# Optimization experiments

Measured on AMD Instinct MI355X. Metric: run time of the kernel, lower is better.

The kernel has to match this reference:

```python
import jax, jax.numpy as jnp
import numpy as np

ALPHA = 0.2   # LeakyReLU negative slope
NEG = -1e9    # mask value for non-edges


def setup_inputs() -> dict:
    key = jax.random.key(0)
    ks = jax.random.split(key, 8)
    N, Din, F, H, Dout = 4096, 512, 64, 8, 16
    adj = (jax.random.uniform(ks[0], (N, N)) < 0.01).astype(jnp.float32)
    adjacency = jnp.maximum(adj, jnp.eye(N, dtype=jnp.float32))
    X = jax.random.normal(ks[1], (N, Din), jnp.float32)
    s = lambda k, shape, fan: jax.random.normal(k, shape, jnp.float32) / np.float32(np.sqrt(fan))
    W = s(ks[2], (H, Din, F), Din)        # per-head projection, stacked
    a1 = s(ks[3], (H, F), F)              # attention vector, source half
    a2 = s(ks[4], (H, F), F)              # attention vector, target half
    Wo = s(ks[5], (H * F, Dout), H * F)   # output-layer projection
    ao1 = s(ks[6], (Dout,), Dout)
    ao2 = s(ks[7], (Dout,), Dout)
    return dict(adjacency=adjacency, X=X, W=W, a1=a1, a2=a2, Wo=Wo, ao1=ao1, ao2=ao2)


def reference(adjacency, X, W, a1, a2, Wo, ao1, ao2):
    # dropout is identity (eval mode / p=0)
    mask = adjacency > 0
    N = X.shape[0]
    # --- multi-head attention layers (concat=True -> ELU) ---
    Wh = jnp.einsum('nd,hdf->hnf', X, W)                      # [H, N, F]
    f1 = jnp.einsum('hnf,hf->hn', Wh, a1)                     # [H, N]
    f2 = jnp.einsum('hnf,hf->hn', Wh, a2)                     # [H, N]
    e = jax.nn.leaky_relu(f1[:, :, None] + f2[:, None, :], ALPHA)  # [H, N, N]
    att = jax.nn.softmax(jnp.where(mask[None], e, NEG), axis=-1)
    heads = jax.nn.elu(jnp.einsum('hnm,hmf->hnf', att, Wh))   # [H, N, F]
    cat = jnp.transpose(heads, (1, 0, 2)).reshape(N, -1)      # [N, H*F]
    # --- output attention layer (concat=False -> no ELU) ---
    Who = cat @ Wo                                            # [N, Dout]
    eo = jax.nn.leaky_relu((Who @ ao1)[:, None] + (Who @ ao2)[None, :], ALPHA)
    atto = jax.nn.softmax(jnp.where(mask, eo, NEG), axis=-1)  # [N, N]
    return atto @ Who                                         # [N, Dout]
```

## Files before the change

kernel.cpp:

```cpp
#include <hip/hip_runtime.h>
#include <hip/hip_bf16.h>

#define N_NODES 4096
#define DIN     512
#define FDIM    64
#define NHEADS  8
#define DOUT    16
#define MAXN    512

typedef __attribute__((ext_vector_type(8))) short bf16x8;
typedef __attribute__((ext_vector_type(4))) float f32x4;

static __device__ __forceinline__ float us2f(unsigned short u) {
    union { unsigned int i; float f; } cv; cv.i = ((unsigned int)u) << 16; return cv.f;
}
static __device__ __forceinline__ unsigned short f2us(float v) {
    __hip_bfloat16 b = __float2bfloat16(v);
    return *(const unsigned short*)&b;
}
static __device__ __forceinline__ int is_f32(const void* adj) {
    return (((const unsigned short*)adj)[0] == 0) ? 1 : 0;
}

__global__ __launch_bounds__(256) void prep_nbr_kernel(
    const void* __restrict__ adj, const void* __restrict__ X, const void* __restrict__ W,
    const void* __restrict__ a1, const void* __restrict__ a2, const void* __restrict__ Wo,
    const void* __restrict__ ao1, const void* __restrict__ ao2,
    unsigned short* __restrict__ Xb, unsigned short* __restrict__ Wt,
    unsigned short* __restrict__ WtH, unsigned short* __restrict__ WtL,
    float* __restrict__ a1c, float* __restrict__ a2c,
    float* __restrict__ ao1c, float* __restrict__ ao2c,
    int* __restrict__ cnt, int* __restrict__ nbr)
{
    const int f32 = is_f32(adj);
    if (blockIdx.x >= 1024) {
        const int n = blockIdx.x - 1024;
        __shared__ int c;
        if (threadIdx.x == 0) c = 0;
        __syncthreads();
        if (f32) {
            const uint4* row = (const uint4*)((const unsigned int*)adj + (size_t)n * N_NODES);
            for (int q = threadIdx.x; q < N_NODES / 4; q += 256) {
                uint4 v = row[q];
                int base = q * 4;
                if (v.x) { int p = atomicAdd(&c, 1); if (p < MAXN) nbr[(size_t)n * MAXN + p] = base + 0; }
                if (v.y) { int p = atomicAdd(&c, 1); if (p < MAXN) nbr[(size_t)n * MAXN + p] = base + 1; }
                if (v.z) { int p = atomicAdd(&c, 1); if (p < MAXN) nbr[(size_t)n * MAXN + p] = base + 2; }
                if (v.w) { int p = atomicAdd(&c, 1); if (p < MAXN) nbr[(size_t)n * MAXN + p] = base + 3; }
            }
        } else {
            const ushort4* row = (const ushort4*)((const unsigned short*)adj + (size_t)n * N_NODES);
            for (int q = threadIdx.x; q < N_NODES / 4; q += 256) {
                ushort4 v = row[q];
                int base = q * 4;
                if (v.x) { int p = atomicAdd(&c, 1); if (p < MAXN) nbr[(size_t)n * MAXN + p] = base + 0; }
                if (v.y) { int p = atomicAdd(&c, 1); if (p < MAXN) nbr[(size_t)n * MAXN + p] = base + 1; }
                if (v.z) { int p = atomicAdd(&c, 1); if (p < MAXN) nbr[(size_t)n * MAXN + p] = base + 2; }
                if (v.w) { int p = atomicAdd(&c, 1); if (p < MAXN) nbr[(size_t)n * MAXN + p] = base + 3; }
            }
        }
        __syncthreads();
        if (threadIdx.x == 0) cnt[n] = (c < MAXN) ? c : MAXN;
        return;
    }
    const int i0 = blockIdx.x * 256 + threadIdx.x;
    const int T = 1024 * 256;
    for (int i = i0; i < N_NODES * DIN; i += T) {
        float v = f32 ? ((const float*)X)[i] : us2f(((const unsigned short*)X)[i]);
        Xb[i] = f2us(v);
    }
    for (int i = i0; i < NHEADS * DIN * FDIM; i += T) {
        int hh = i >> 15, rem = i & 32767, d = rem >> 6, f = rem & 63;
        float v = f32 ? ((const float*)W)[i] : us2f(((const unsigned short*)W)[i]);
        Wt[((size_t)(hh * FDIM + f)) * DIN + d] = f2us(v);
    }
    for (int i = i0; i < DIN * DOUT; i += T) {
        int d = i >> 4, j = i & 15;
        float v = f32 ? ((const float*)Wo)[i] : us2f(((const unsigned short*)Wo)[i]);
        unsigned short hi = f2us(v);
        WtH[j * DIN + d] = hi;
        WtL[j * DIN + d] = f2us(v - us2f(hi));
    }
    if (i0 < 512) {
        a1c[i0] = f32 ? ((const float*)a1)[i0] : us2f(((const unsigned short*)a1)[i0]);
        a2c[i0] = f32 ? ((const float*)a2)[i0] : us2f(((const unsigned short*)a2)[i0]);
    }
    if (i0 < 16) {
        ao1c[i0] = f32 ? ((const float*)ao1)[i0] : us2f(((const unsigned short*)ao1)[i0]);
        ao2c[i0] = f32 ? ((const float*)ao2)[i0] : us2f(((const unsigned short*)ao2)[i0]);
    }
}

__global__ __launch_bounds__(256) void wh_f12_kernel(
    const unsigned short* __restrict__ Xb, const unsigned short* __restrict__ Wt,
    const float* __restrict__ a1c, const float* __restrict__ a2c,
    unsigned short* __restrict__ Whb, float* __restrict__ f1, float* __restrict__ f2)
{
    const int h  = blockIdx.x;
    const int bm = blockIdx.y;
    const int w    = threadIdx.x >> 6;
    const int lane = threadIdx.x & 63;
    const int quad = lane >> 4;
    const int l16  = lane & 15;
    const int rowA = bm * 64 + w * 16 + l16;

    f32x4 acc[4];
#pragma unroll
    for (int j = 0; j < 4; ++j) acc[j] = (f32x4){0.f, 0.f, 0.f, 0.f};

    const unsigned short* xp = Xb + (size_t)rowA * DIN + quad * 8;
    const unsigned short* wb = Wt + (size_t)h * FDIM * DIN + quad * 8;
#pragma unroll 4
    for (int k0 = 0; k0 < DIN; k0 += 32) {
        bf16x8 a = *(const bf16x8*)(xp + k0);
#pragma unroll
        for (int j = 0; j < 4; ++j) {
            bf16x8 b = *(const bf16x8*)(wb + (size_t)(j * 16 + l16) * DIN + k0);
            acc[j] = __builtin_amdgcn_mfma_f32_16x16x32_bf16(a, b, acc[j], 0, 0, 0);
        }
    }
    float av1[4], av2[4];
#pragma unroll
    for (int j = 0; j < 4; ++j) {
        int col = j * 16 + l16;
        av1[j] = a1c[h * FDIM + col];
        av2[j] = a2c[h * FDIM + col];
#pragma unroll
        for (int rr = 0; rr < 4; ++rr) {
            int row = bm * 64 + w * 16 + quad * 4 + rr;
            Whb[((size_t)row * NHEADS + h) * FDIM + col] = f2us(acc[j][rr]);
        }
    }
#pragma unroll
    for (int rr = 0; rr < 4; ++rr) {
        float p1 = acc[0][rr] * av1[0] + acc[1][rr] * av1[1] + acc[2][rr] * av1[2] + acc[3][rr] * av1[3];
        float p2 = acc[0][rr] * av2[0] + acc[1][rr] * av2[1] + acc[2][rr] * av2[2] + acc[3][rr] * av2[3];
#pragma unroll
        for (int off = 8; off; off >>= 1) {
            p1 += __shfl_xor(p1, off);
            p2 += __shfl_xor(p2, off);
        }
        if (l16 == 0) {
            int row = bm * 64 + w * 16 + quad * 4 + rr;
            f1[h * N_NODES + row] = p1;
            f2[h * N_NODES + row] = p2;
        }
    }
}

__global__ __launch_bounds__(256) void attn1_kernel(
    const unsigned short* __restrict__ Whb,
    const float* __restrict__ f1, const float* __restrict__ f2,
    const int* __restrict__ cnt, const int* __restrict__ nbr,
    unsigned short* __restrict__ catb)
{
    const int n = blockIdx.x;
    const int tid = threadIdx.x;
    __shared__ int sh_m[MAXN];
    __shared__ float sh_s[NHEADS][516];
    __shared__ float sh_inv[NHEADS];
    const int c0 = cnt[n];
    const int c = (c0 < MAXN) ? c0 : MAXN;
    for (int k = tid; k < c; k += 256) sh_m[k] = nbr[(size_t)n * MAXN + k];
    __syncthreads();
    const int h = tid >> 5;
    const int l32 = tid & 31;
    const float f1v = f1[h * N_NODES + n];
    float mx = -1e30f;
    for (int k = l32; k < c; k += 32) {
        float s = f1v + f2[h * N_NODES + sh_m[k]];
        s = (s >= 0.f) ? s : 0.2f * s;
        sh_s[h][k] = s;
        mx = fmaxf(mx, s);
    }
#pragma unroll
    for (int off = 16; off; off >>= 1) mx = fmaxf(mx, __shfl_xor(mx, off));
    __syncthreads();
    float sum = 0.f;
    for (int k = l32; k < c; k += 32) {
        float e = __expf(sh_s[h][k] - mx);
        sh_s[h][k] = e;
        sum += e;
    }
#pragma unroll
    for (int off = 16; off; off >>= 1) sum += __shfl_xor(sum, off);
    if (l32 == 0) sh_inv[h] = (sum > 0.f) ? 1.f / sum : 0.f;
    __syncthreads();
    float a0 = 0.f, a1v = 0.f;
    const unsigned int* base = (const unsigned int*)Whb;
#pragma unroll 8
    for (int k = 0; k < c; ++k) {
        unsigned int u = base[(size_t)sh_m[k] * 256 + tid];
        float wgt = sh_s[h][k];
        a0  += wgt * us2f((unsigned short)(u & 0xFFFFu));
        a1v += wgt * us2f((unsigned short)(u >> 16));
    }
    const float inv = sh_inv[h];
    a0 *= inv; a1v *= inv;
    a0  = (a0  > 0.f) ? a0  : expm1f(a0);
    a1v = (a1v > 0.f) ? a1v : expm1f(a1v);
    unsigned int o = (unsigned int)f2us(a0) | ((unsigned int)f2us(a1v) << 16);
    ((unsigned int*)catb)[(size_t)n * 256 + tid] = o;
}

__global__ __launch_bounds__(64) void who_mfma_g_kernel(
    const unsigned short* __restrict__ catb,
    const unsigned short* __restrict__ WtH, const unsigned short* __restrict__ WtL,
    const float* __restrict__ ao1c, const float* __restrict__ ao2c,
    float* __restrict__ Who, float* __restrict__ g1, float* __restrict__ g2)
{
    const int lane = threadIdx.x;
    const int quad = lane >> 4, l16 = lane & 15;
    const int row0 = blockIdx.x * 16;
    f32x4 acc = (f32x4){0.f, 0.f, 0.f, 0.f};
    for (int k0 = 0; k0 < DIN; k0 += 32) {
        bf16x8 a  = *(const bf16x8*)&catb[(size_t)(row0 + l16) * DIN + k0 + quad * 8];
        bf16x8 bh = *(const bf16x8*)&WtH[l16 * DIN + k0 + quad * 8];
        bf16x8 bl = *(const bf16x8*)&WtL[l16 * DIN + k0 + quad * 8];
        acc = __builtin_amdgcn_mfma_f32_16x16x32_bf16(a, bh, acc, 0, 0, 0);
        acc = __builtin_amdgcn_mfma_f32_16x16x32_bf16(a, bl, acc, 0, 0, 0);
    }
#pragma unroll
    for (int rr = 0; rr < 4; ++rr) {
        int row = row0 + quad * 4 + rr;
        float v = acc[rr];
        Who[row * DOUT + l16] = v;
        float p1 = v * ao1c[l16];
        float p2 = v * ao2c[l16];
#pragma unroll
        for (int off = 8; off; off >>= 1) {
            p1 += __shfl_xor(p1, off);
            p2 += __shfl_xor(p2, off);
        }
        if (l16 == 0) { g1[row] = p1; g2[row] = p2; }
    }
}

__global__ __launch_bounds__(64) void attn2_kernel(
    const void* __restrict__ adj,
    const float* __restrict__ Who,
    const float* __restrict__ g1, const float* __restrict__ g2,
    const int* __restrict__ cnt, const int* __restrict__ nbr,
    void* __restrict__ out)
{
    const int n = blockIdx.x;
    const int lane = threadIdx.x;
    const int quad = lane >> 4, l16 = lane & 15;
    __shared__ float sh_s[MAXN];
    __shared__ int sh_m[MAXN];
    const int c0 = cnt[n];
    const int c = (c0 < MAXN) ? c0 : MAXN;
    for (int k = lane; k < c; k += 64) sh_m[k] = nbr[(size_t)n * MAXN + k];
    __syncthreads();
    const float gn = g1[n];
    float mx = -1e30f;
    for (int k = lane; k < c; k += 64) {
        float s = gn + g2[sh_m[k]];
        s = (s >= 0.f) ? s : 0.2f * s;
        sh_s[k] = s;
        mx = fmaxf(mx, s);
    }
#pragma unroll
    for (int off = 32; off; off >>= 1) mx = fmaxf(mx, __shfl_xor(mx, off));
    __syncthreads();
    float sum = 0.f;
    for (int k = lane; k < c; k += 64) {
        float e = __expf(sh_s[k] - mx);
        sh_s[k] = e;
        sum += e;
    }
#pragma unroll
    for (int off = 32; off; off >>= 1) sum += __shfl_xor(sum, off);
    __syncthreads();
    const float inv = (sum > 0.f) ? 1.f / sum : 0.f;
    float accv = 0.f;
#pragma unroll 4
    for (int k = quad; k < c; k += 4)
        accv += sh_s[k] * Who[sh_m[k] * DOUT + l16];
    accv += __shfl_xor(accv, 16);
    accv += __shfl_xor(accv, 32);
    if (quad == 0) {
        float v = accv * inv;
        if (is_f32(adj)) ((float*)out)[n * DOUT + l16] = v;
        else             ((unsigned short*)out)[n * DOUT + l16] = f2us(v);
    }
}

__global__ void wsfail_kernel(float* __restrict__ out)
{
    if (threadIdx.x == 0) out[0] = 129.f;
}

extern "C" void kernel_launch(void* const* d_in, const int* in_sizes, int n_in,
                              void* d_out, int out_size, void* d_ws, size_t ws_size,
                              hipStream_t stream)
{
    const void* adj = d_in[0];
    const void* X   = d_in[1];
    const void* W   = d_in[2];
    const void* a1  = d_in[3];
    const void* a2  = d_in[4];
    const void* Wo  = d_in[5];
    const void* ao1 = d_in[6];
    const void* ao2 = d_in[7];

    const size_t NEEDED = 22000000;
    if (ws_size < NEEDED) { wsfail_kernel<<<1, 64, 0, stream>>>((float*)d_out); return; }

    int*   cnt  = (int*)d_ws;
    int*   nbr  = cnt + 4096;
    float* a1c  = (float*)(nbr + 2097152);
    float* a2c  = a1c + 512;
    float* ao1c = a2c + 512;
    float* ao2c = ao1c + 16;
    float* f1   = ao2c + 16;
    float* f2   = f1 + 32768;
    float* Who  = f2 + 32768;
    float* g1   = Who + 65536;
    float* g2   = g1 + 4096;
    unsigned short* Whb  = (unsigned short*)(g2 + 4096);
    unsigned short* catb = Whb + 2097152;
    unsigned short* Xb   = catb + 2097152;
    unsigned short* Wt   = Xb + 2097152;
    unsigned short* WtH  = Wt + 262144;
    unsigned short* WtL  = WtH + 8192;

    prep_nbr_kernel<<<1024 + N_NODES, 256, 0, stream>>>(
        adj, X, W, a1, a2, Wo, ao1, ao2,
        Xb, Wt, WtH, WtL, a1c, a2c, ao1c, ao2c, cnt, nbr);
    wh_f12_kernel<<<dim3(NHEADS, N_NODES / 64), 256, 0, stream>>>(
        Xb, Wt, a1c, a2c, Whb, f1, f2);
    attn1_kernel<<<N_NODES, 256, 0, stream>>>(Whb, f1, f2, cnt, nbr, catb);
    who_mfma_g_kernel<<<N_NODES / 16, 64, 0, stream>>>(catb, WtH, WtL, ao1c, ao2c, Who, g1, g2);
    attn2_kernel<<<N_NODES, 64, 0, stream>>>(adj, Who, g1, g2, cnt, nbr, d_out);
}
```

Baseline: 162.4 us.

## Fuse neighbor scan, head aggregation and output projection into attention kernel

Moves the per-row adjacency scan out of the prep kernel and into the first attention kernel, which keeps the neighbor list in shared memory and writes it out for the second layer. The output projection (cat @ Wo plus the g1/g2 dot products) is now done per node inside the same kernel in fp32, which removes the catb round trip and the separate MFMA kernel. The aggregation loop is restructured so each wave handles a different neighbor and loads 16-byte vectors, followed by a cross-wave shared-memory reduction. The wh_f12 MFMA operands are swapped so each lane stores contiguous features with a vector store. The fused kernel gains shared memory and a scalar per-node projection that may lower occupancy.

```diff
diff --git a/kernel.cpp b/kernel.cpp
--- a/kernel.cpp
+++ b/kernel.cpp
@@ -22,47 +22,16 @@
     return (((const unsigned short*)adj)[0] == 0) ? 1 : 0;
 }
 
-__global__ __launch_bounds__(256) void prep_nbr_kernel(
+__global__ __launch_bounds__(256) void prep_kernel(
     const void* __restrict__ adj, const void* __restrict__ X, const void* __restrict__ W,
     const void* __restrict__ a1, const void* __restrict__ a2, const void* __restrict__ Wo,
     const void* __restrict__ ao1, const void* __restrict__ ao2,
     unsigned short* __restrict__ Xb, unsigned short* __restrict__ Wt,
-    unsigned short* __restrict__ WtH, unsigned short* __restrict__ WtL,
+    float* __restrict__ Woc,
     float* __restrict__ a1c, float* __restrict__ a2c,
-    float* __restrict__ ao1c, float* __restrict__ ao2c,
-    int* __restrict__ cnt, int* __restrict__ nbr)
+    float* __restrict__ ao1c, float* __restrict__ ao2c)
 {
     const int f32 = is_f32(adj);
-    if (blockIdx.x >= 1024) {
-        const int n = blockIdx.x - 1024;
-        __shared__ int c;
-        if (threadIdx.x == 0) c = 0;
-        __syncthreads();
-        if (f32) {
-            const uint4* row = (const uint4*)((const unsigned int*)adj + (size_t)n * N_NODES);
-            for (int q = threadIdx.x; q < N_NODES / 4; q += 256) {
-                uint4 v = row[q];
-                int base = q * 4;
-                if (v.x) { int p = atomicAdd(&c, 1); if (p < MAXN) nbr[(size_t)n * MAXN + p] = base + 0; }
-                if (v.y) { int p = atomicAdd(&c, 1); if (p < MAXN) nbr[(size_t)n * MAXN + p] = base + 1; }
-                if (v.z) { int p = atomicAdd(&c, 1); if (p < MAXN) nbr[(size_t)n * MAXN + p] = base + 2; }
-                if (v.w) { int p = atomicAdd(&c, 1); if (p < MAXN) nbr[(size_t)n * MAXN + p] = base + 3; }
-            }
-        } else {
-            const ushort4* row = (const ushort4*)((const unsigned short*)adj + (size_t)n * N_NODES);
-            for (int q = threadIdx.x; q < N_NODES / 4; q += 256) {
-                ushort4 v = row[q];
-                int base = q * 4;
-                if (v.x) { int p = atomicAdd(&c, 1); if (p < MAXN) nbr[(size_t)n * MAXN + p] = base + 0; }
-                if (v.y) { int p = atomicAdd(&c, 1); if (p < MAXN) nbr[(size_t)n * MAXN + p] = base + 1; }
-                if (v.z) { int p = atomicAdd(&c, 1); if (p < MAXN) nbr[(size_t)n * MAXN + p] = base + 2; }
-                if (v.w) { int p = atomicAdd(&c, 1); if (p < MAXN) nbr[(size_t)n * MAXN + p] = base + 3; }
-            }
-        }
-        __syncthreads();
-        if (threadIdx.x == 0) cnt[n] = (c < MAXN) ? c : MAXN;
-        return;
-    }
     const int i0 = blockIdx.x * 256 + threadIdx.x;
     const int T = 1024 * 256;
     for (int i = i0; i < N_NODES * DIN; i += T) {
@@ -74,12 +43,9 @@
         float v = f32 ? ((const float*)W)[i] : us2f(((const unsigned short*)W)[i]);
         Wt[((size_t)(hh * FDIM + f)) * DIN + d] = f2us(v);
     }
-    for (int i = i0; i < DIN * DOUT; i += T) {
-        int d = i >> 4, j = i & 15;
-        float v = f32 ? ((const float*)Wo)[i] : us2f(((const unsigned short*)Wo)[i]);
-        unsigned short hi = f2us(v);
-        WtH[j * DIN + d] = hi;
-        WtL[j * DIN + d] = f2us(v - us2f(hi));
+    if (i0 < DIN * DOUT) {
+        float v = f32 ? ((const float*)Wo)[i0] : us2f(((const unsigned short*)Wo)[i0]);
+        Woc[i0] = v;
     }
     if (i0 < 512) {
         a1c[i0] = f32 ? ((const float*)a1)[i0] : us2f(((const unsigned short*)a1)[i0]);
@@ -102,67 +68,97 @@
     const int lane = threadIdx.x & 63;
     const int quad = lane >> 4;
     const int l16  = lane & 15;
-    const int rowA = bm * 64 + w * 16 + l16;
+    const int node = bm * 64 + w * 16 + l16;
 
     f32x4 acc[4];
 #pragma unroll
     for (int j = 0; j < 4; ++j) acc[j] = (f32x4){0.f, 0.f, 0.f, 0.f};
 
-    const unsigned short* xp = Xb + (size_t)rowA * DIN + quad * 8;
-    const unsigned short* wb = Wt + (size_t)h * FDIM * DIN + quad * 8;
+    const unsigned short* xp = Xb + (size_t)node * DIN + quad * 8;
+    const unsigned short* wp = Wt + (size_t)h * FDIM * DIN + quad * 8;
 #pragma unroll 4
     for (int k0 = 0; k0 < DIN; k0 += 32) {
-        bf16x8 a = *(const bf16x8*)(xp + k0);
+        bf16x8 b = *(const bf16x8*)(xp + k0);
 #pragma unroll
         for (int j = 0; j < 4; ++j) {
-            bf16x8 b = *(const bf16x8*)(wb + (size_t)(j * 16 + l16) * DIN + k0);
+            bf16x8 a = *(const bf16x8*)(wp + (size_t)(j * 16 + l16) * DIN + k0);
             acc[j] = __builtin_amdgcn_mfma_f32_16x16x32_bf16(a, b, acc[j], 0, 0, 0);
         }
     }
-    float av1[4], av2[4];
+    float p1 = 0.f, p2 = 0.f;
 #pragma unroll
     for (int j = 0; j < 4; ++j) {
-        int col = j * 16 + l16;
-        av1[j] = a1c[h * FDIM + col];
-        av2[j] = a2c[h * FDIM + col];
+        const int fbase = j * 16 + quad * 4;
+        ushort4 st;
+        st.x = f2us(acc[j][0]); st.y = f2us(acc[j][1]);
+        st.z = f2us(acc[j][2]); st.w = f2us(acc[j][3]);
+        *(ushort4*)&Whb[((size_t)node * NHEADS + h) * FDIM + fbase] = st;
 #pragma unroll
         for (int rr = 0; rr < 4; ++rr) {
-            int row = bm * 64 + w * 16 + quad * 4 + rr;
-            Whb[((size_t)row * NHEADS + h) * FDIM + col] = f2us(acc[j][rr]);
-        }
-    }
-#pragma unroll
-    for (int rr = 0; rr < 4; ++rr) {
-        float p1 = acc[0][rr] * av1[0] + acc[1][rr] * av1[1] + acc[2][rr] * av1[2] + acc[3][rr] * av1[3];
-        float p2 = acc[0][rr] * av2[0] + acc[1][rr] * av2[1] + acc[2][rr] * av2[2] + acc[3][rr] * av2[3];
-#pragma unroll
-        for (int off = 8; off; off >>= 1) {
-            p1 += __shfl_xor(p1, off);
-            p2 += __shfl_xor(p2, off);
-        }
-        if (l16 == 0) {
-            int row = bm * 64 + w * 16 + quad * 4 + rr;
-            f1[h * N_NODES + row] = p1;
-            f2[h * N_NODES + row] = p2;
-        }
-    }
-}
-
-__global__ __launch_bounds__(256) void attn1_kernel(
+            p1 += acc[j][rr] * a1c[h * FDIM + fbase + rr];
+            p2 += acc[j][rr] * a2c[h * FDIM + fbase + rr];
+        }
+    }
+    p1 += __shfl_xor(p1, 16); p1 += __shfl_xor(p1, 32);
+    p2 += __shfl_xor(p2, 16); p2 += __shfl_xor(p2, 32);
+    if (quad == 0) {
+        f1[h * N_NODES + node] = p1;
+        f2[h * N_NODES + node] = p2;
+    }
+}
+
+__global__ __launch_bounds__(256) void attn1_fused_kernel(
+    const void* __restrict__ adj,
     const unsigned short* __restrict__ Whb,
     const float* __restrict__ f1, const float* __restrict__ f2,
-    const int* __restrict__ cnt, const int* __restrict__ nbr,
-    unsigned short* __restrict__ catb)
-{
-    const int n = blockIdx.x;
+    const float* __restrict__ Woc,
+    const float* __restrict__ ao1c, const float* __restrict__ ao2c,
+    int* __restrict__ cnt, int* __restrict__ nbr,
+    float* __restrict__ Who, float* __restrict__ g1, float* __restrict__ g2)
+{
+    const int n   = blockIdx.x;
     const int tid = threadIdx.x;
-    __shared__ int sh_m[MAXN];
+    const int wv  = tid >> 6;
+    const int lane = tid & 63;
+
+    __shared__ int   sh_m[MAXN];
+    __shared__ int   sh_c;
     __shared__ float sh_s[NHEADS][516];
     __shared__ float sh_inv[NHEADS];
-    const int c0 = cnt[n];
-    const int c = (c0 < MAXN) ? c0 : MAXN;
-    for (int k = tid; k < c; k += 256) sh_m[k] = nbr[(size_t)n * MAXN + k];
-    __syncthreads();
+    __shared__ float sh_red[3][64][9];
+    __shared__ float cat_sh[512];
+    __shared__ float sh_p[16 * 17];
+
+    if (tid == 0) sh_c = 0;
+    __syncthreads();
+    if (is_f32(adj)) {
+        const uint4* row = (const uint4*)((const unsigned int*)adj + (size_t)n * N_NODES);
+#pragma unroll 4
+        for (int q = tid; q < N_NODES / 4; q += 256) {
+            uint4 v = row[q];
+            int base = q * 4;
+            if (v.x) { int p = atomicAdd(&sh_c, 1); if (p < MAXN) sh_m[p] = base + 0; }
+            if (v.y) { int p = atomicAdd(&sh_c, 1); if (p < MAXN) sh_m[p] = base + 1; }
+            if (v.z) { int p = atomicAdd(&sh_c, 1); if (p < MAXN) sh_m[p] = base + 2; }
+            if (v.w) { int p = atomicAdd(&sh_c, 1); if (p < MAXN) sh_m[p] = base + 3; }
+        }
+    } else {
+        const ushort4* row = (const ushort4*)((const unsigned short*)adj + (size_t)n * N_NODES);
+#pragma unroll 4
+        for (int q = tid; q < N_NODES / 4; q += 256) {
+            ushort4 v = row[q];
+            int base = q * 4;
+            if (v.x) { int p = atomicAdd(&sh_c, 1); if (p < MAXN) sh_m[p] = base + 0; }
+            if (v.y) { int p = atomicAdd(&sh_c, 1); if (p < MAXN) sh_m[p] = base + 1; }
+            if (v.z) { int p = atomicAdd(&sh_c, 1); if (p < MAXN) sh_m[p] = base + 2; }
+            if (v.w) { int p = atomicAdd(&sh_c, 1); if (p < MAXN) sh_m[p] = base + 3; }
+        }
+    }
+    __syncthreads();
+    const int c = (sh_c < MAXN) ? sh_c : MAXN;
+    for (int k = tid; k < c; k += 256) nbr[(size_t)n * MAXN + k] = sh_m[k];
+    if (tid == 0) cnt[n] = c;
+
     const int h = tid >> 5;
     const int l32 = tid & 31;
     const float f1v = f1[h * N_NODES + n];
@@ -175,7 +171,6 @@
     }
 #pragma unroll
     for (int off = 16; off; off >>= 1) mx = fmaxf(mx, __shfl_xor(mx, off));
-    __syncthreads();
     float sum = 0.f;
     for (int k = l32; k < c; k += 32) {
         float e = __expf(sh_s[h][k] - mx);
@@ -186,53 +181,66 @@
     for (int off = 16; off; off >>= 1) sum += __shfl_xor(sum, off);
     if (l32 == 0) sh_inv[h] = (sum > 0.f) ? 1.f / sum : 0.f;
     __syncthreads();
-    float a0 = 0.f, a1v = 0.f;
-    const unsigned int* base = (const unsigned int*)Whb;
-#pragma unroll 8
-    for (int k = 0; k < c; ++k) {
-        unsigned int u = base[(size_t)sh_m[k] * 256 + tid];
-        float wgt = sh_s[h][k];
-        a0  += wgt * us2f((unsigned short)(u & 0xFFFFu));
-        a1v += wgt * us2f((unsigned short)(u >> 16));
-    }
-    const float inv = sh_inv[h];
-    a0 *= inv; a1v *= inv;
-    a0  = (a0  > 0.f) ? a0  : expm1f(a0);
-    a1v = (a1v > 0.f) ? a1v : expm1f(a1v);
-    unsigned int o = (unsigned int)f2us(a0) | ((unsigned int)f2us(a1v) << 16);
-    ((unsigned int*)catb)[(size_t)n * 256 + tid] = o;
-}
-
-__global__ __launch_bounds__(64) void who_mfma_g_kernel(
-    const unsigned short* __restrict__ catb,
-    const unsigned short* __restrict__ WtH, const unsigned short* __restrict__ WtL,
-    const float* __restrict__ ao1c, const float* __restrict__ ao2c,
-    float* __restrict__ Who, float* __restrict__ g1, float* __restrict__ g2)
-{
-    const int lane = threadIdx.x;
-    const int quad = lane >> 4, l16 = lane & 15;
-    const int row0 = blockIdx.x * 16;
-    f32x4 acc = (f32x4){0.f, 0.f, 0.f, 0.f};
-    for (int k0 = 0; k0 < DIN; k0 += 32) {
-        bf16x8 a  = *(const bf16x8*)&catb[(size_t)(row0 + l16) * DIN + k0 + quad * 8];
-        bf16x8 bh = *(const bf16x8*)&WtH[l16 * DIN + k0 + quad * 8];
-        bf16x8 bl = *(const bf16x8*)&WtL[l16 * DIN + k0 + quad * 8];
-        acc = __builtin_amdgcn_mfma_f32_16x16x32_bf16(a, bh, acc, 0, 0, 0);
-        acc = __builtin_amdgcn_mfma_f32_16x16x32_bf16(a, bl, acc, 0, 0, 0);
-    }
-#pragma unroll
-    for (int rr = 0; rr < 4; ++rr) {
-        int row = row0 + quad * 4 + rr;
-        float v = acc[rr];
-        Who[row * DOUT + l16] = v;
-        float p1 = v * ao1c[l16];
-        float p2 = v * ao2c[l16];
+
+    const int hh = lane >> 3;
+    float acc8[8];
+#pragma unroll
+    for (int e = 0; e < 8; ++e) acc8[e] = 0.f;
+    const uint4* wb = (const uint4*)Whb;
+#pragma unroll 2
+    for (int kb = 0; kb < c; kb += 4) {
+        const int k = kb + wv;
+        float wgt = 0.f; int m = sh_m[0];
+        if (k < c) { wgt = sh_s[hh][k]; m = sh_m[k]; }
+        uint4 v = wb[(size_t)m * 64 + lane];
+        acc8[0] += wgt * us2f((unsigned short)(v.x & 0xFFFFu));
+        acc8[1] += wgt * us2f((unsigned short)(v.x >> 16));
+        acc8[2] += wgt * us2f((unsigned short)(v.y & 0xFFFFu));
+        acc8[3] += wgt * us2f((unsigned short)(v.y >> 16));
+        acc8[4] += wgt * us2f((unsigned short)(v.z & 0xFFFFu));
+        acc8[5] += wgt * us2f((unsigned short)(v.z >> 16));
+        acc8[6] += wgt * us2f((unsigned short)(v.w & 0xFFFFu));
+        acc8[7] += wgt * us2f((unsigned short)(v.w >> 16));
+    }
+    if (wv) {
+#pragma unroll
+        for (int e = 0; e < 8; ++e) sh_red[wv - 1][lane][e] = acc8[e];
+    }
+    __syncthreads();
+    if (wv == 0) {
+        const float inv = sh_inv[hh];
+#pragma unroll
+        for (int e = 0; e < 8; ++e) {
+            float s = acc8[e] + sh_red[0][lane][e] + sh_red[1][lane][e] + sh_red[2][lane][e];
+            s *= inv;
+            s = (s > 0.f) ? s : expm1f(s);
+            cat_sh[lane * 8 + e] = s;
+        }
+    }
+    __syncthreads();
+
+    {
+        const int j = tid & 15, ch = tid >> 4;
+        float s = 0.f;
+#pragma unroll
+        for (int d = 0; d < 32; ++d)
+            s += cat_sh[ch * 32 + d] * Woc[(ch * 32 + d) * DOUT + j];
+        sh_p[ch * 17 + j] = s;
+    }
+    __syncthreads();
+    if (tid < 16) {
+        float s = 0.f;
+#pragma unroll
+        for (int ch = 0; ch < 16; ++ch) s += sh_p[ch * 17 + tid];
+        Who[n * DOUT + tid] = s;
+        float p1 = s * ao1c[tid];
+        float p2 = s * ao2c[tid];
 #pragma unroll
         for (int off = 8; off; off >>= 1) {
             p1 += __shfl_xor(p1, off);
             p2 += __shfl_xor(p2, off);
         }
-        if (l16 == 0) { g1[row] = p1; g2[row] = p2; }
+        if (tid == 0) { g1[n] = p1; g2[n] = p2; }
     }
 }
 
@@ -318,19 +326,17 @@
     float* Who  = f2 + 32768;
     float* g1   = Who + 65536;
     float* g2   = g1 + 4096;
-    unsigned short* Whb  = (unsigned short*)(g2 + 4096);
-    unsigned short* catb = Whb + 2097152;
-    unsigned short* Xb   = catb + 2097152;
-    unsigned short* Wt   = Xb + 2097152;
-    unsigned short* WtH  = Wt + 262144;
-    unsigned short* WtL  = WtH + 8192;
-
-    prep_nbr_kernel<<<1024 + N_NODES, 256, 0, stream>>>(
+    float* Woc  = g2 + 4096;
+    unsigned short* Whb = (unsigned short*)(Woc + 8192);
+    unsigned short* Xb  = Whb + 2097152;
+    unsigned short* Wt  = Xb + 2097152;
+
+    prep_kernel<<<1024, 256, 0, stream>>>(
         adj, X, W, a1, a2, Wo, ao1, ao2,
-        Xb, Wt, WtH, WtL, a1c, a2c, ao1c, ao2c, cnt, nbr);
+        Xb, Wt, Woc, a1c, a2c, ao1c, ao2c);
     wh_f12_kernel<<<dim3(NHEADS, N_NODES / 64), 256, 0, stream>>>(
         Xb, Wt, a1c, a2c, Whb, f1, f2);
-    attn1_kernel<<<N_NODES, 256, 0, stream>>>(Whb, f1, f2, cnt, nbr, catb);
-    who_mfma_g_kernel<<<N_NODES / 16, 64, 0, stream>>>(catb, WtH, WtL, ao1c, ao2c, Who, g1, g2);
+    attn1_fused_kernel<<<N_NODES, 256, 0, stream>>>(
+        adj, Whb, f1, f2, Woc, ao1c, ao2c, cnt, nbr, Who, g1, g2);
     attn2_kernel<<<N_NODES, 64, 0, stream>>>(adj, Who, g1, g2, cnt, nbr, d_out);
 }
```

New measurement: 174.2 us. 7.3% more time.
